# Kernel optimization log

Hardware: AMD Instinct MI355X
Metric: run time of the kernel (lower is better)

Reference implementation:

```python
import jax, jax.numpy as jnp
import numpy as np

# ---- static config (model_cfg equivalents) ----
H_GRIDS, W_GRIDS = 2, 2
S_TOKENS = 1024          # H*W with H=W=32
C_DIM = 768
NUM_HEADS = 12
D_HEAD = 64
TOKEN_SIZE = (24, 24)    # model_cfg.token_size
SCALE = 1.0
BETA = 1.2               # model_cfg.beta (token_norm path)
GAMMA = 3.0              # model_cfg.gamma
CUTTING_HP = 0.1         # model_cfg.cutting_hp
TEMPERATURE = 0.07       # model_cfg.temperature
N_CLUSTERS = 32


def _l2norm(x, eps=1e-12):
    # matches torch F.normalize(dim=-1)
    n = jnp.linalg.norm(x, axis=-1, keepdims=True)
    return x / jnp.maximum(n, eps)


def setup_inputs() -> dict:
    key = jax.random.key(0)
    k1, k2, k3 = jax.random.split(key, 3)
    B = H_GRIDS * W_GRIDS
    ex = jax.random.normal(k1, (H_GRIDS, W_GRIDS, S_TOKENS, C_DIM), jnp.float32)
    indices = jax.random.randint(k2, (B * S_TOKENS,), 0, N_CLUSTERS)
    v_ext = jax.random.normal(k3, (B * NUM_HEADS, TOKEN_SIZE[0], TOKEN_SIZE[1], D_HEAD), jnp.float32)
    return {"ex_feats_grid": ex, "v_ext": v_ext, "indices": indices}


def _forward(ex_feats_grid, v_ext, indices):
    hg, wg, S, C = ex_feats_grid.shape
    B = hg * wg
    H = W = int(S ** 0.5)
    N = B * S
    x = ex_feats_grid.reshape(N, C)                          # [N, C]
    nh = v_ext.shape[0] // B
    Dh = v_ext.shape[-1]

    # --- value branch: bilinear resize (align_corners=False) to (H, W) ---
    v = v_ext.transpose(0, 3, 1, 2)                          # [B*nh, Dh, t0, t1]
    v = jax.image.resize(v, (B * nh, Dh, H, W), method='bilinear')
    v = v.reshape(B, nh, Dh, S).transpose(1, 0, 3, 2).reshape(nh, N, Dh)  # [nh, N, Dh]

    # --- proxy candidate mask: same cluster label OR 8-neighbor within same grid block ---
    indices_mask = indices[:, None] == indices[None, :]       # [N, N]
    rr, cc = jnp.meshgrid(jnp.arange(H), jnp.arange(W), indexing='ij')
    coords = jnp.stack([rr.ravel(), cc.ravel()], axis=1)      # [S, 2]
    delta = coords[:, None, :] - coords[None, :, :]           # [S, S, 2]
    window = (jnp.max(jnp.abs(delta), axis=-1) <= 1) & (jnp.sum(jnp.abs(delta), axis=-1) > 0)
    blk = jnp.arange(N) // S
    neighbor = (blk[:, None] == blk[None, :]) & jnp.tile(window, (B, B))  # block_diag(window x B)
    cand = indices_mask | neighbor                            # [N, N]

    count = jnp.maximum(cand.sum(-1, keepdims=True), 1).astype(x.dtype)
    proxy = (cand.astype(x.dtype) @ x) / count                # [N, C] averaged proxy feats

    key_feats = _l2norm(x)
    attn = _l2norm(proxy) @ key_feats.T                       # [N, N] proxy similarity (mini_iters=0)
    attn = attn.reshape(B, S, N) * SCALE

    # --- token_norm rescale (static beta/gamma) ---
    sim_mean = jnp.maximum(attn.mean(-1, keepdims=True), 0.0)  # sim_mean[sim_mean<0]=0
    attn = (attn - sim_mean * BETA) * GAMMA

    # --- dynamic threshold cut + masked softmax ---
    cut = jnp.minimum(attn.max(-1, keepdims=True), CUTTING_HP)
    attn = jnp.where(attn < cut, -jnp.inf, attn)
    attn = jax.nn.softmax(attn / TEMPERATURE, axis=-1)        # each row keeps >=1 finite entry

    out = jnp.einsum('bsn,hnd->hsbd', attn, v)                # [nh, S, B, Dh]
    return out.transpose(1, 2, 0, 3).reshape(S, B, nh * Dh)   # [S, B, nh*Dh]


def reference(ex_feats_grid, v_ext, indices):
    return _forward(ex_feats_grid, v_ext, indices)
```

## Files before the change

### kernel.cpp

```cpp
#include <hip/hip_runtime.h>
#include <hip/hip_bf16.h>
#include <stdint.h>

typedef __attribute__((ext_vector_type(8))) short    bf16x8;
typedef __attribute__((ext_vector_type(4))) float    f32x4;
typedef __attribute__((ext_vector_type(8))) unsigned short u16x8;
typedef __attribute__((ext_vector_type(8))) _Float16 f16x8;

#define N_TOK   4096
#define C_DIM   768
#define NCLU    32
#define ZSPLIT  8

__device__ __forceinline__ uint16_t f2bf(float f){
  union { float f; unsigned u; } v; v.f = f;
  unsigned r = v.u + 0x7fffu + ((v.u >> 16) & 1u);
  return (uint16_t)(r >> 16);
}

__device__ __forceinline__ void gl2lds16(const void* g, void* l){
  __builtin_amdgcn_global_load_lds(
      (const __attribute__((address_space(1))) unsigned int*)g,
      (__attribute__((address_space(3))) unsigned int*)l, 16, 0, 0);
}

__global__ __launch_bounds__(256) void csum_part_k(const float* __restrict__ x, const int* __restrict__ idx,
                                                   float* __restrict__ part){
  __shared__ float lacc[NCLU * 256];
  __shared__ int   sidx[32];
  const int tc = blockIdx.x, chunk = blockIdx.y;
  const int tid = threadIdx.x;
  #pragma unroll
  for (int u = 0; u < NCLU; ++u) lacc[u * 256 + tid] = 0.f;
  if (tid < 32) sidx[tid] = idx[tc * 32 + tid];
  __syncthreads();
  const int ch = chunk * 256 + tid;
  const float* xb = x + (size_t)(tc * 32) * C_DIM + ch;
  #pragma unroll 8
  for (int t = 0; t < 32; ++t){
    int c = sidx[t];
    lacc[c * 256 + tid] += xb[(size_t)t * C_DIM];
  }
  __syncthreads();
  float* pb = part + ((size_t)tc * NCLU) * C_DIM + chunk * 256 + tid;
  #pragma unroll
  for (int c = 0; c < NCLU; ++c) pb[(size_t)c * C_DIM] = lacc[c * 256 + tid];
}

__global__ __launch_bounds__(256) void csum_red_k(const float* __restrict__ part, float* __restrict__ csum){
  const int t = blockIdx.x * 256 + threadIdx.x;
  float acc = 0.f;
  #pragma unroll 8
  for (int tc = 0; tc < 128; ++tc) acc += part[(size_t)tc * (NCLU * C_DIM) + t];
  csum[t] = acc;
}

__global__ __launch_bounds__(256) void proxy_key_k(const float* __restrict__ x, const int* __restrict__ idx,
                                                   const float* __restrict__ csum,
                                                   uint16_t* __restrict__ An, uint16_t* __restrict__ Bn){
  __shared__ float red[8];
  const int i = blockIdx.x, tid = threadIdx.x;
  const int ci = idx[i];
  const int b = i >> 10, s = i & 1023, r = s >> 5, w = s & 31;
  const int drs[8] = {-1,-1,-1, 0, 0, 1, 1, 1};
  const int dws[8] = {-1, 0, 1,-1, 1,-1, 0, 1};
  int js[8]; unsigned mask = 0;
  #pragma unroll
  for (int t = 0; t < 8; ++t){
    int rr = r + drs[t], ww = w + dws[t];
    bool ok = ((unsigned)rr < 32u) && ((unsigned)ww < 32u);
    int j = (b << 10) + (rr << 5) + ww;
    js[t] = ok ? j : i;
    if (ok && idx[js[t]] != ci) mask |= (1u << t);
  }
  float xs[3], ps[3]; float ssx = 0.f, ssp = 0.f;
  #pragma unroll
  for (int u = 0; u < 3; ++u){
    int ch = tid + u * 256;
    float xv = x[(size_t)i * C_DIM + ch];
    float pv = csum[ci * C_DIM + ch];
    #pragma unroll
    for (int t = 0; t < 8; ++t)
      if (mask & (1u << t)) pv += x[(size_t)js[t] * C_DIM + ch];
    xs[u] = xv; ps[u] = pv;
    ssx += xv * xv; ssp += pv * pv;
  }
  for (int m = 32; m; m >>= 1){ ssx += __shfl_xor(ssx, m); ssp += __shfl_xor(ssp, m); }
  const int wid = tid >> 6;
  if ((tid & 63) == 0){ red[wid] = ssx; red[4 + wid] = ssp; }
  __syncthreads();
  ssx = red[0] + red[1] + red[2] + red[3];
  ssp = red[4] + red[5] + red[6] + red[7];
  float rnx = 1.f / fmaxf(sqrtf(ssx), 1e-12f);
  float rnp = 1.f / fmaxf(sqrtf(ssp), 1e-12f);
  #pragma unroll
  for (int u = 0; u < 3; ++u){
    int ch = tid + u * 256;
    Bn[(size_t)i * C_DIM + ch] = f2bf(xs[u] * rnx);
    An[(size_t)i * C_DIM + ch] = f2bf(ps[u] * rnp);
  }
}

template<int MODE>
__global__ __launch_bounds__(256) void gemm_bt_k(const uint16_t* __restrict__ A, const uint16_t* __restrict__ B,
                                                 int ldA, int ldB, int K,
                                                 _Float16* __restrict__ Sout,
                                                 const float* __restrict__ rden,
                                                 _Float16* __restrict__ Obuf,
                                                 const float* __restrict__ vext,
                                                 uint16_t* __restrict__ Vt){
  __shared__ __align__(16) char smem[32768];
  const int g = blockIdx.x;
  const int tid = threadIdx.x;

  if (MODE == 0 && g >= 1024){
    float* ld = (float*)smem;
    const int rb = g - 1024, bh = rb >> 5, y = rb & 31;
    const int b = bh / 12, h = bh % 12;
    const float* base = vext + (size_t)bh * 576 * 64;
    float sy = (y + 0.5f) * 0.75f - 0.5f;
    float fy0 = floorf(sy); float fy = sy - fy0; int y0 = (int)fy0;
    int iy0 = y0 < 0 ? 0 : y0;  int iy1 = (y0 + 1 > 23) ? 23 : y0 + 1;
    const int d = tid & 63, xg = tid >> 6;
    #pragma unroll
    for (int jj = 0; jj < 8; ++jj){
      int xx = xg + 4 * jj;
      float sx = (xx + 0.5f) * 0.75f - 0.5f;
      float fx0 = floorf(sx); float fx = sx - fx0; int x0 = (int)fx0;
      int ix0 = x0 < 0 ? 0 : x0;  int ix1 = (x0 + 1 > 23) ? 23 : x0 + 1;
      float v00 = base[(iy0 * 24 + ix0) * 64 + d];
      float v01 = base[(iy0 * 24 + ix1) * 64 + d];
      float v10 = base[(iy1 * 24 + ix0) * 64 + d];
      float v11 = base[(iy1 * 24 + ix1) * 64 + d];
      ld[d * 33 + xx] = (1.f - fy) * ((1.f - fx) * v00 + fx * v01)
                      +        fy  * ((1.f - fx) * v10 + fx * v11);
    }
    __syncthreads();
    const int xx = tid & 31, dg = tid >> 5;
    const int n = b * 1024 + y * 32 + xx;
    #pragma unroll
    for (int jj = 0; jj < 8; ++jj){
      int d2 = dg * 8 + jj;
      Vt[(size_t)(h * 64 + d2) * 4096 + n] = f2bf(ld[d2 * 33 + xx]);
    }
    return;
  }

  const int lane = tid & 63, wid = tid >> 6;
  const int q = lane >> 4, l16 = lane & 15;
  const int wrow = wid & 1, wcol = wid >> 1;

  const int xcd = g & 7;
  const int j   = g >> 3;
  int i0, n0, kt0, per, z = 0;
  const int KT = K >> 6;
  if (MODE == 0){
    int sq = j >> 4;
    int mi = ((sq >> 2) << 2) + ((j >> 2) & 3);
    int ni = ((sq & 3) << 2) + (j & 3);
    i0 = (((xcd >> 1) << 3) + mi) * 128;
    n0 = (((xcd & 1) << 4) + ni) * 128;
    kt0 = 0; per = KT;
  } else {
    z  = xcd;
    i0 = (j / 6) * 128;
    n0 = (j % 6) * 128;
    per = KT >> 3; kt0 = z * per;
  }

  f32x4 acc[4][4] = {};

  for (int kt = kt0; kt < kt0 + per; ++kt){
    const int k0 = kt << 6;
    #pragma unroll
    for (int t = 0; t < 4; ++t){
      int p   = t * 256 + tid;
      int row = p >> 3, kc = p & 7;
      int kcs = kc ^ (row & 7);
      gl2lds16(A + (size_t)(i0 + row) * ldA + k0 + kcs * 8, smem + p * 16);
      gl2lds16(B + (size_t)(n0 + row) * ldB + k0 + kcs * 8, smem + 16384 + p * 16);
    }
    __syncthreads();
    #pragma unroll
    for (int ks = 0; ks < 2; ++ks){
      bf16x8 af[4], bfr[4];
      #pragma unroll
      for (int mt = 0; mt < 4; ++mt){
        int row = wrow * 64 + mt * 16 + l16;
        int ck  = (ks * 4 + q) ^ (row & 7);
        af[mt] = *(const bf16x8*)(smem + row * 128 + ck * 16);
      }
      #pragma unroll
      for (int nt = 0; nt < 4; ++nt){
        int row = wcol * 64 + nt * 16 + l16;
        int ck  = (ks * 4 + q) ^ (row & 7);
        bfr[nt] = *(const bf16x8*)(smem + 16384 + row * 128 + ck * 16);
      }
      #pragma unroll
      for (int mt = 0; mt < 4; ++mt)
        #pragma unroll
        for (int nt = 0; nt < 4; ++nt)
          acc[mt][nt] = __builtin_amdgcn_mfma_f32_16x16x32_bf16(af[mt], bfr[nt], acc[mt][nt], 0, 0, 0);
    }
    __syncthreads();
  }

  _Float16* Pz = (MODE == 1) ? (Obuf + (size_t)z * N_TOK * C_DIM) : nullptr;
  #pragma unroll
  for (int mt = 0; mt < 4; ++mt){
    #pragma unroll
    for (int r = 0; r < 4; ++r){
      int row = i0 + wrow * 64 + mt * 16 + q * 4 + r;
      float rd = (MODE == 1) ? rden[row] : 0.f;
      #pragma unroll
      for (int nt = 0; nt < 4; ++nt){
        int col = n0 + wcol * 64 + nt * 16 + l16;
        float v = acc[mt][nt][r];
        if (MODE == 0)
          Sout[(size_t)row * 4096 + col] = (_Float16)v;
        else
          Pz[(size_t)row * C_DIM + col] = (_Float16)(v * rd);
      }
    }
  }
}

__global__ __launch_bounds__(256) void rowsoftmax_k(const _Float16* __restrict__ S, uint16_t* __restrict__ P,
                                                    float* __restrict__ rden){
  __shared__ float red[8];
  const int row = blockIdx.x, tid = threadIdx.x;
  const f16x8* Sr = (const f16x8*)(S + (size_t)row * 4096);
  f16x8 h0 = Sr[tid], h1 = Sr[256 + tid];
  float v[16];
  float mx = -3.4e38f, sm = 0.f;
  #pragma unroll
  for (int e = 0; e < 8; ++e){ v[e] = (float)h0[e]; v[8 + e] = (float)h1[e]; }
  #pragma unroll
  for (int e = 0; e < 16; ++e){ mx = fmaxf(mx, v[e]); sm += v[e]; }
  for (int m = 32; m; m >>= 1){ mx = fmaxf(mx, __shfl_xor(mx, m)); sm += __shfl_xor(sm, m); }
  const int wid = tid >> 6;
  if ((tid & 63) == 0){ red[wid] = mx; red[4 + wid] = sm; }
  __syncthreads();
  mx = fmaxf(fmaxf(red[0], red[1]), fmaxf(red[2], red[3]));
  sm = red[4] + red[5] + red[6] + red[7];

  float bmu  = 1.2f * fmaxf(sm * (1.f / 4096.f), 0.f);
  float amax = 3.0f * (mx - bmu);
  float cut  = fminf(amax, 0.1f);

  float den = 0.f; uint16_t pv[16];
  #pragma unroll
  for (int e = 0; e < 16; ++e){
    float a  = 3.0f * (v[e] - bmu);
    float ev = (a >= cut) ? __expf((a - amax) * (1.f / 0.07f)) : 0.f;
    den += ev;
    pv[e] = f2bf(ev);
  }
  for (int m = 32; m; m >>= 1) den += __shfl_xor(den, m);
  __syncthreads();
  if ((tid & 63) == 0) red[wid] = den;
  __syncthreads();
  den = red[0] + red[1] + red[2] + red[3];
  if (tid == 0) rden[row] = 1.f / den;

  u16x8* Pr = (u16x8*)(P + (size_t)row * 4096);
  u16x8 o0, o1;
  #pragma unroll
  for (int e = 0; e < 8; ++e){ o0[e] = pv[e]; o1[e] = pv[8 + e]; }
  Pr[tid] = o0; Pr[256 + tid] = o1;
}

__global__ __launch_bounds__(256) void reduce_k(const _Float16* __restrict__ Pz, float* __restrict__ out){
  const int t = blockIdx.x * 256 + threadIdx.x;
  const int row = t / 96, c8 = t % 96;
  const size_t base = (size_t)row * C_DIM + c8 * 8;
  const size_t zs = (size_t)N_TOK * C_DIM;
  float o[8] = {0.f, 0.f, 0.f, 0.f, 0.f, 0.f, 0.f, 0.f};
  #pragma unroll
  for (int z = 0; z < ZSPLIT; ++z){
    f16x8 a = *(const f16x8*)(Pz + base + (size_t)z * zs);
    #pragma unroll
    for (int e = 0; e < 8; ++e) o[e] += (float)a[e];
  }
  const int s = row & 1023, bb = row >> 10;
  float* dst = out + (size_t)s * 3072 + bb * 768 + c8 * 8;
  ((float4*)dst)[0] = make_float4(o[0], o[1], o[2], o[3]);
  ((float4*)dst)[1] = make_float4(o[4], o[5], o[6], o[7]);
}

extern "C" void kernel_launch(void* const* d_in, const int* in_sizes, int n_in,
                              void* d_out, int out_size, void* d_ws, size_t ws_size,
                              hipStream_t stream){
  (void)in_sizes; (void)n_in; (void)out_size; (void)ws_size;
  const float* ex   = (const float*)d_in[0];
  const float* vext = (const float*)d_in[1];
  const int*   idx  = (const int*)d_in[2];
  float* out = (float*)d_out;
  char* ws = (char*)d_ws;

  uint16_t* P    = (uint16_t*)(ws);
  float*    part = (float*)(ws);
  uint16_t* Vt   = (uint16_t*)(ws + 33554432);
  char*     R    = ws + 39845888;
  uint16_t* An   = (uint16_t*)(R);
  uint16_t* Bn   = (uint16_t*)(R + 6291456);
  _Float16* S16  = (_Float16*)(R + 12582912);
  _Float16* Pz   = (_Float16*)(R);
  float*    csum = (float*)(ws + 90177536);
  float*    rden = (float*)(ws + 90275840);

  csum_part_k<<<dim3(128, 3), 256, 0, stream>>>(ex, idx, part);
  csum_red_k<<<96, 256, 0, stream>>>(part, csum);
  proxy_key_k<<<N_TOK, 256, 0, stream>>>(ex, idx, csum, An, Bn);
  gemm_bt_k<0><<<2560, 256, 0, stream>>>(An, Bn, 768, 768, 768, S16, nullptr, nullptr, vext, Vt);
  rowsoftmax_k<<<N_TOK, 256, 0, stream>>>(S16, P, rden);
  gemm_bt_k<1><<<1536, 256, 0, stream>>>(P, Vt, 4096, 4096, 4096, nullptr, rden, Pz, nullptr, nullptr);
  reduce_k<<<1536, 256, 0, stream>>>(Pz, out);
}
```

Measured before the change: 200.8 us.

## Use atomic cluster sums and wave-per-row proxy and softmax kernels

Replaces the two-pass cluster-sum (partials then reduction kernel) with a memset plus atomicAdd accumulation into the cluster sums, which removes one launch and the partial buffer traffic. The proxy/key normalization and row softmax kernels now assign one wavefront per row, using float4/f16x8 vector loads and shuffle-only reductions with no shared memory or block barriers. Atomics make the float summation order nondeterministic, and the wave-per-row softmax holds 64 floats per lane, which raises register pressure.

```diff
diff --git a/kernel.cpp b/kernel.cpp
--- a/kernel.cpp
+++ b/kernel.cpp
@@ -5,6 +5,7 @@
 typedef __attribute__((ext_vector_type(8))) short    bf16x8;
 typedef __attribute__((ext_vector_type(4))) float    f32x4;
 typedef __attribute__((ext_vector_type(8))) unsigned short u16x8;
+typedef __attribute__((ext_vector_type(4))) unsigned short u16x4;
 typedef __attribute__((ext_vector_type(8))) _Float16 f16x8;
 
 #define N_TOK   4096
@@ -25,7 +26,7 @@
 }
 
 __global__ __launch_bounds__(256) void csum_part_k(const float* __restrict__ x, const int* __restrict__ idx,
-                                                   float* __restrict__ part){
+                                                   float* __restrict__ csum){
   __shared__ float lacc[NCLU * 256];
   __shared__ int   sidx[32];
   const int tc = blockIdx.x, chunk = blockIdx.y;
@@ -42,24 +43,16 @@
     lacc[c * 256 + tid] += xb[(size_t)t * C_DIM];
   }
   __syncthreads();
-  float* pb = part + ((size_t)tc * NCLU) * C_DIM + chunk * 256 + tid;
-  #pragma unroll
-  for (int c = 0; c < NCLU; ++c) pb[(size_t)c * C_DIM] = lacc[c * 256 + tid];
-}
-
-__global__ __launch_bounds__(256) void csum_red_k(const float* __restrict__ part, float* __restrict__ csum){
-  const int t = blockIdx.x * 256 + threadIdx.x;
-  float acc = 0.f;
-  #pragma unroll 8
-  for (int tc = 0; tc < 128; ++tc) acc += part[(size_t)tc * (NCLU * C_DIM) + t];
-  csum[t] = acc;
+  float* cb = csum + chunk * 256 + tid;
+  #pragma unroll
+  for (int c = 0; c < NCLU; ++c) atomicAdd(cb + (size_t)c * C_DIM, lacc[c * 256 + tid]);
 }
 
 __global__ __launch_bounds__(256) void proxy_key_k(const float* __restrict__ x, const int* __restrict__ idx,
                                                    const float* __restrict__ csum,
                                                    uint16_t* __restrict__ An, uint16_t* __restrict__ Bn){
-  __shared__ float red[8];
-  const int i = blockIdx.x, tid = threadIdx.x;
+  const int i = blockIdx.x * 4 + (threadIdx.x >> 6);
+  const int lane = threadIdx.x & 63;
   const int ci = idx[i];
   const int b = i >> 10, s = i & 1023, r = s >> 5, w = s & 31;
   const int drs[8] = {-1,-1,-1, 0, 0, 1, 1, 1};
@@ -73,31 +66,40 @@
     js[t] = ok ? j : i;
     if (ok && idx[js[t]] != ci) mask |= (1u << t);
   }
-  float xs[3], ps[3]; float ssx = 0.f, ssp = 0.f;
+  const float4* xr = (const float4*)(x + (size_t)i * C_DIM);
+  const float4* cr = (const float4*)(csum + (size_t)ci * C_DIM);
+  float4 xs[3], ps[3]; float ssx = 0.f, ssp = 0.f;
   #pragma unroll
   for (int u = 0; u < 3; ++u){
-    int ch = tid + u * 256;
-    float xv = x[(size_t)i * C_DIM + ch];
-    float pv = csum[ci * C_DIM + ch];
+    int c4 = u * 64 + lane;
+    float4 xv = xr[c4];
+    float4 pv = cr[c4];
     #pragma unroll
     for (int t = 0; t < 8; ++t)
-      if (mask & (1u << t)) pv += x[(size_t)js[t] * C_DIM + ch];
+      if (mask & (1u << t)){
+        float4 nv = ((const float4*)(x + (size_t)js[t] * C_DIM))[c4];
+        pv.x += nv.x; pv.y += nv.y; pv.z += nv.z; pv.w += nv.w;
+      }
     xs[u] = xv; ps[u] = pv;
-    ssx += xv * xv; ssp += pv * pv;
-  }
+    ssx += xv.x*xv.x + xv.y*xv.y + xv.z*xv.z + xv.w*xv.w;
+    ssp += pv.x*pv.x + pv.y*pv.y + pv.z*pv.z + pv.w*pv.w;
+  }
+  #pragma unroll
   for (int m = 32; m; m >>= 1){ ssx += __shfl_xor(ssx, m); ssp += __shfl_xor(ssp, m); }
-  const int wid = tid >> 6;
-  if ((tid & 63) == 0){ red[wid] = ssx; red[4 + wid] = ssp; }
-  __syncthreads();
-  ssx = red[0] + red[1] + red[2] + red[3];
-  ssp = red[4] + red[5] + red[6] + red[7];
   float rnx = 1.f / fmaxf(sqrtf(ssx), 1e-12f);
   float rnp = 1.f / fmaxf(sqrtf(ssp), 1e-12f);
+  u16x4* Br = (u16x4*)(Bn + (size_t)i * C_DIM);
+  u16x4* Ar = (u16x4*)(An + (size_t)i * C_DIM);
   #pragma unroll
   for (int u = 0; u < 3; ++u){
-    int ch = tid + u * 256;
-    Bn[(size_t)i * C_DIM + ch] = f2bf(xs[u] * rnx);
-    An[(size_t)i * C_DIM + ch] = f2bf(ps[u] * rnp);
+    int c4 = u * 64 + lane;
+    u16x4 ob, oa;
+    ob[0] = f2bf(xs[u].x * rnx); ob[1] = f2bf(xs[u].y * rnx);
+    ob[2] = f2bf(xs[u].z * rnx); ob[3] = f2bf(xs[u].w * rnx);
+    oa[0] = f2bf(ps[u].x * rnp); oa[1] = f2bf(ps[u].y * rnp);
+    oa[2] = f2bf(ps[u].z * rnp); oa[3] = f2bf(ps[u].w * rnp);
+    Br[c4] = ob;
+    Ar[c4] = oa;
   }
 }
 
@@ -227,47 +229,46 @@
 
 __global__ __launch_bounds__(256) void rowsoftmax_k(const _Float16* __restrict__ S, uint16_t* __restrict__ P,
                                                     float* __restrict__ rden){
-  __shared__ float red[8];
-  const int row = blockIdx.x, tid = threadIdx.x;
+  const int row = blockIdx.x * 4 + (threadIdx.x >> 6);
+  const int lane = threadIdx.x & 63;
   const f16x8* Sr = (const f16x8*)(S + (size_t)row * 4096);
-  f16x8 h0 = Sr[tid], h1 = Sr[256 + tid];
-  float v[16];
+  f16x8 h[8];
+  #pragma unroll
+  for (int c = 0; c < 8; ++c) h[c] = Sr[c * 64 + lane];
+  float v[64];
   float mx = -3.4e38f, sm = 0.f;
   #pragma unroll
-  for (int e = 0; e < 8; ++e){ v[e] = (float)h0[e]; v[8 + e] = (float)h1[e]; }
-  #pragma unroll
-  for (int e = 0; e < 16; ++e){ mx = fmaxf(mx, v[e]); sm += v[e]; }
+  for (int c = 0; c < 8; ++c)
+    #pragma unroll
+    for (int e = 0; e < 8; ++e){
+      float f = (float)h[c][e];
+      v[c * 8 + e] = f; mx = fmaxf(mx, f); sm += f;
+    }
+  #pragma unroll
   for (int m = 32; m; m >>= 1){ mx = fmaxf(mx, __shfl_xor(mx, m)); sm += __shfl_xor(sm, m); }
-  const int wid = tid >> 6;
-  if ((tid & 63) == 0){ red[wid] = mx; red[4 + wid] = sm; }
-  __syncthreads();
-  mx = fmaxf(fmaxf(red[0], red[1]), fmaxf(red[2], red[3]));
-  sm = red[4] + red[5] + red[6] + red[7];
 
   float bmu  = 1.2f * fmaxf(sm * (1.f / 4096.f), 0.f);
   float amax = 3.0f * (mx - bmu);
   float cut  = fminf(amax, 0.1f);
 
-  float den = 0.f; uint16_t pv[16];
-  #pragma unroll
-  for (int e = 0; e < 16; ++e){
-    float a  = 3.0f * (v[e] - bmu);
-    float ev = (a >= cut) ? __expf((a - amax) * (1.f / 0.07f)) : 0.f;
-    den += ev;
-    pv[e] = f2bf(ev);
-  }
+  float den = 0.f;
+  u16x8 o[8];
+  #pragma unroll
+  for (int c = 0; c < 8; ++c)
+    #pragma unroll
+    for (int e = 0; e < 8; ++e){
+      float a  = 3.0f * (v[c * 8 + e] - bmu);
+      float ev = (a >= cut) ? __expf((a - amax) * (1.f / 0.07f)) : 0.f;
+      den += ev;
+      o[c][e] = f2bf(ev);
+    }
+  #pragma unroll
   for (int m = 32; m; m >>= 1) den += __shfl_xor(den, m);
-  __syncthreads();
-  if ((tid & 63) == 0) red[wid] = den;
-  __syncthreads();
-  den = red[0] + red[1] + red[2] + red[3];
-  if (tid == 0) rden[row] = 1.f / den;
+  if (lane == 0) rden[row] = 1.f / den;
 
   u16x8* Pr = (u16x8*)(P + (size_t)row * 4096);
-  u16x8 o0, o1;
-  #pragma unroll
-  for (int e = 0; e < 8; ++e){ o0[e] = pv[e]; o1[e] = pv[8 + e]; }
-  Pr[tid] = o0; Pr[256 + tid] = o1;
+  #pragma unroll
+  for (int c = 0; c < 8; ++c) Pr[c * 64 + lane] = o[c];
 }
 
 __global__ __launch_bounds__(256) void reduce_k(const _Float16* __restrict__ Pz, float* __restrict__ out){
@@ -299,7 +300,6 @@
   char* ws = (char*)d_ws;
 
   uint16_t* P    = (uint16_t*)(ws);
-  float*    part = (float*)(ws);
   uint16_t* Vt   = (uint16_t*)(ws + 33554432);
   char*     R    = ws + 39845888;
   uint16_t* An   = (uint16_t*)(R);
@@ -309,11 +309,11 @@
   float*    csum = (float*)(ws + 90177536);
   float*    rden = (float*)(ws + 90275840);
 
-  csum_part_k<<<dim3(128, 3), 256, 0, stream>>>(ex, idx, part);
-  csum_red_k<<<96, 256, 0, stream>>>(part, csum);
-  proxy_key_k<<<N_TOK, 256, 0, stream>>>(ex, idx, csum, An, Bn);
+  hipMemsetAsync(csum, 0, NCLU * C_DIM * sizeof(float), stream);
+  csum_part_k<<<dim3(128, 3), 256, 0, stream>>>(ex, idx, csum);
+  proxy_key_k<<<1024, 256, 0, stream>>>(ex, idx, csum, An, Bn);
   gemm_bt_k<0><<<2560, 256, 0, stream>>>(An, Bn, 768, 768, 768, S16, nullptr, nullptr, vext, Vt);
-  rowsoftmax_k<<<N_TOK, 256, 0, stream>>>(S16, P, rden);
+  rowsoftmax_k<<<1024, 256, 0, stream>>>(S16, P, rden);
   gemm_bt_k<1><<<1536, 256, 0, stream>>>(P, Vt, 4096, 4096, 4096, nullptr, rden, Pz, nullptr, nullptr);
   reduce_k<<<1536, 256, 0, stream>>>(Pz, out);
 }
```

After: 191.3 us. 1.05x faster.
